# Optimization experiments

Measured on AMD Instinct MI355X. Metric: run time of the kernel, lower is better.

The kernel has to match this reference:

```python
import jax, jax.numpy as jnp
import numpy as np

B, S, H = 64, 2048, 1024

def setup_inputs() -> dict:
    key = jax.random.key(0)
    k1, k2 = jax.random.split(key)
    enc_output = jax.random.normal(k1, (B, S, H), dtype=jnp.float32)
    h_n = jax.random.normal(k2, (B, H), dtype=jnp.float32)
    return {"enc_output": enc_output, "h_n": h_n}

def reference(enc_output, h_n):
    # dec_output: [B, 1, H]
    dec_output = h_n[:, None, :]
    # scores: [B, 1, S] = dec_output @ enc_output^T
    scores = jnp.einsum('bqh,bsh->bqs', dec_output, enc_output)
    attn = jax.nn.softmax(scores, axis=2)  # softmax over S
    # context: [B, 1, H] = attn @ enc_output
    context = jnp.einsum('bqs,bsh->bqh', attn, enc_output)
    # concat decoder state and attention context: [B, 1, 2H]
    return jnp.concatenate((dec_output, context), axis=2)
```

## Files before the change

### kernel.cpp

```cpp
#include <hip/hip_runtime.h>
#include <math.h>


#define BB 64
#define SS 2048
#define HH 1024
#define NCHUNK 16
#define SCHUNK (SS / NCHUNK)
#define NWAVE 4

#define WS_ML_OFF ((size_t)BB * NCHUNK * HH)

__global__ __launch_bounds__(256) void attn_partial_kernel(
    const float* __restrict__ enc, const float* __restrict__ hn,
    float* __restrict__ ws)
{
    const int blk   = blockIdx.x;
    const int b     = blk / NCHUNK;
    const int chunk = blk % NCHUNK;
    const int tid   = threadIdx.x;
    const int wave  = tid >> 6;
    const int lane  = tid & 63;

    const float4* hn4 = (const float4*)(hn + (size_t)b * HH);
    float4 h4[4];
#pragma unroll
    for (int j = 0; j < 4; ++j) h4[j] = hn4[j * 64 + lane];

    const float4* enc4 = (const float4*)(enc + (size_t)b * SS * HH);

    float m = -INFINITY;
    float l = 0.0f;
    float4 acc[4];
#pragma unroll
    for (int j = 0; j < 4; ++j) acc[j] = make_float4(0.f, 0.f, 0.f, 0.f);

    const int s0 = chunk * SCHUNK;
    for (int s = s0 + wave; s < s0 + SCHUNK; s += NWAVE) {
        const float4* row = enc4 + (size_t)s * (HH / 4);
        float4 e[4];
#pragma unroll
        for (int j = 0; j < 4; ++j) e[j] = row[j * 64 + lane];

        float d = 0.0f;
#pragma unroll
        for (int j = 0; j < 4; ++j) {
            d += e[j].x * h4[j].x + e[j].y * h4[j].y
               + e[j].z * h4[j].z + e[j].w * h4[j].w;
        }
#pragma unroll
        for (int off = 32; off > 0; off >>= 1)
            d += __shfl_xor(d, off, 64);

        const float m_new = fmaxf(m, d);
        const float scale = __expf(m - m_new);
        const float p     = __expf(d - m_new);
        l = l * scale + p;
#pragma unroll
        for (int j = 0; j < 4; ++j) {
            acc[j].x = acc[j].x * scale + p * e[j].x;
            acc[j].y = acc[j].y * scale + p * e[j].y;
            acc[j].z = acc[j].z * scale + p * e[j].z;
            acc[j].w = acc[j].w * scale + p * e[j].w;
        }
        m = m_new;
    }

    __shared__ float s_m[NWAVE];
    __shared__ float s_l[NWAVE];
    __shared__ float s_acc[NWAVE][HH];

#pragma unroll
    for (int j = 0; j < 4; ++j)
        ((float4*)s_acc[wave])[j * 64 + lane] = acc[j];
    if (lane == 0) { s_m[wave] = m; s_l[wave] = l; }
    __syncthreads();

    float M = fmaxf(fmaxf(s_m[0], s_m[1]), fmaxf(s_m[2], s_m[3]));
    float sc[NWAVE];
    float L = 0.0f;
#pragma unroll
    for (int w = 0; w < NWAVE; ++w) {
        sc[w] = __expf(s_m[w] - M);
        L += s_l[w] * sc[w];
    }

    float4 ctx = make_float4(0.f, 0.f, 0.f, 0.f);
#pragma unroll
    for (int w = 0; w < NWAVE; ++w) {
        float4 a = ((const float4*)s_acc[w])[tid];
        ctx.x += sc[w] * a.x;  ctx.y += sc[w] * a.y;
        ctx.z += sc[w] * a.z;  ctx.w += sc[w] * a.w;
    }
    ((float4*)(ws + (size_t)blk * HH))[tid] = ctx;
    if (tid == 0) {
        ws[WS_ML_OFF + (size_t)blk * 2 + 0] = M;
        ws[WS_ML_OFF + (size_t)blk * 2 + 1] = L;
    }
}

__global__ __launch_bounds__(256) void attn_final_kernel(
    const float* __restrict__ hn, const float* __restrict__ ws,
    float* __restrict__ out)
{
    const int b   = blockIdx.x;
    const int tid = threadIdx.x;
    const float* ml = ws + WS_ML_OFF + (size_t)b * NCHUNK * 2;

    float M = -INFINITY;
#pragma unroll
    for (int c = 0; c < NCHUNK; ++c) M = fmaxf(M, ml[c * 2]);

    float sc[NCHUNK];
    float T = 0.0f;
#pragma unroll
    for (int c = 0; c < NCHUNK; ++c) {
        sc[c] = __expf(ml[c * 2] - M);
        T += sc[c] * ml[c * 2 + 1];
    }
    const float invT = 1.0f / T;

    float4 ctx = make_float4(0.f, 0.f, 0.f, 0.f);
#pragma unroll
    for (int c = 0; c < NCHUNK; ++c) {
        float4 a = ((const float4*)(ws + (size_t)(b * NCHUNK + c) * HH))[tid];
        ctx.x += sc[c] * a.x;  ctx.y += sc[c] * a.y;
        ctx.z += sc[c] * a.z;  ctx.w += sc[c] * a.w;
    }
    ctx.x *= invT; ctx.y *= invT; ctx.z *= invT; ctx.w *= invT;

    const float4 dec = ((const float4*)(hn + (size_t)b * HH))[tid];
    float4* o = (float4*)(out + (size_t)b * 2 * HH);
    o[tid]                = dec;
    o[tid + (HH / 4)]     = ctx;
}

extern "C" void kernel_launch(void* const* d_in, const int* in_sizes, int n_in,
                              void* d_out, int out_size, void* d_ws, size_t ws_size,
                              hipStream_t stream) {
    const float* enc = (const float*)d_in[0];
    const float* hn  = (const float*)d_in[1];
    float* out = (float*)d_out;
    float* ws  = (float*)d_ws;

    attn_partial_kernel<<<dim3(BB * NCHUNK), dim3(256), 0, stream>>>(enc, hn, ws);
    attn_final_kernel<<<dim3(BB), dim3(256), 0, stream>>>(hn, ws, out);
}
```

Measured before the change: 674.6 us.

## Batch four rows per wave in online softmax and double chunk count

Each wave now processes a contiguous run of rows in tiles of four. It issues all four rows' loads together, interleaves the four shuffle reductions, and does one rescale of the accumulator per tile instead of one per row. This is meant to raise memory-level parallelism and shorten the serial dependency chain in this bandwidth-bound kernel. The chunk count doubles to 32, giving 2048 blocks for more occupancy across CUs, at the cost of a larger partial workspace and more work in the final reduction. The extra per-tile registers may lower occupancy.

```diff
diff --git a/kernel.cpp b/kernel.cpp
--- a/kernel.cpp
+++ b/kernel.cpp
@@ -5,9 +5,12 @@
 #define BB 64
 #define SS 2048
 #define HH 1024
-#define NCHUNK 16
+#define NCHUNK 32
 #define SCHUNK (SS / NCHUNK)
 #define NWAVE 4
+#define RPW (SCHUNK / NWAVE)
+#define TT 4
+#define NTILE (RPW / TT)
 
 #define WS_ML_OFF ((size_t)BB * NCHUNK * HH)
 
@@ -35,33 +38,59 @@
 #pragma unroll
     for (int j = 0; j < 4; ++j) acc[j] = make_float4(0.f, 0.f, 0.f, 0.f);
 
-    const int s0 = chunk * SCHUNK;
-    for (int s = s0 + wave; s < s0 + SCHUNK; s += NWAVE) {
-        const float4* row = enc4 + (size_t)s * (HH / 4);
-        float4 e[4];
+    const int ws0 = chunk * SCHUNK + wave * RPW;
+
+    for (int t = 0; t < NTILE; ++t) {
+        const int sbase = ws0 + t * TT;
+
+        float4 e[TT][4];
 #pragma unroll
-        for (int j = 0; j < 4; ++j) e[j] = row[j * 64 + lane];
+        for (int r = 0; r < TT; ++r) {
+            const float4* row = enc4 + (size_t)(sbase + r) * (HH / 4);
+#pragma unroll
+            for (int j = 0; j < 4; ++j) e[r][j] = row[j * 64 + lane];
+        }
 
-        float d = 0.0f;
+        float d[TT];
+#pragma unroll
+        for (int r = 0; r < TT; ++r) {
+            float s = 0.0f;
+#pragma unroll
+            for (int j = 0; j < 4; ++j) {
+                s += e[r][j].x * h4[j].x + e[r][j].y * h4[j].y
+                   + e[r][j].z * h4[j].z + e[r][j].w * h4[j].w;
+            }
+            d[r] = s;
+        }
+
+#pragma unroll
+        for (int off = 32; off > 0; off >>= 1) {
+#pragma unroll
+            for (int r = 0; r < TT; ++r)
+                d[r] += __shfl_xor(d[r], off, 64);
+        }
+
+        float tmax = fmaxf(fmaxf(d[0], d[1]), fmaxf(d[2], d[3]));
+        const float m_new = fmaxf(m, tmax);
+        const float scale = __expf(m - m_new);
+        float p[TT];
+        float psum = 0.0f;
+#pragma unroll
+        for (int r = 0; r < TT; ++r) {
+            p[r] = __expf(d[r] - m_new);
+            psum += p[r];
+        }
+        l = l * scale + psum;
 #pragma unroll
         for (int j = 0; j < 4; ++j) {
-            d += e[j].x * h4[j].x + e[j].y * h4[j].y
-               + e[j].z * h4[j].z + e[j].w * h4[j].w;
-        }
+            float x = acc[j].x * scale, y = acc[j].y * scale;
+            float z = acc[j].z * scale, w = acc[j].w * scale;
 #pragma unroll
-        for (int off = 32; off > 0; off >>= 1)
-            d += __shfl_xor(d, off, 64);
-
-        const float m_new = fmaxf(m, d);
-        const float scale = __expf(m - m_new);
-        const float p     = __expf(d - m_new);
-        l = l * scale + p;
-#pragma unroll
-        for (int j = 0; j < 4; ++j) {
-            acc[j].x = acc[j].x * scale + p * e[j].x;
-            acc[j].y = acc[j].y * scale + p * e[j].y;
-            acc[j].z = acc[j].z * scale + p * e[j].z;
-            acc[j].w = acc[j].w * scale + p * e[j].w;
+            for (int r = 0; r < TT; ++r) {
+                x += p[r] * e[r][j].x;  y += p[r] * e[r][j].y;
+                z += p[r] * e[r][j].z;  w += p[r] * e[r][j].w;
+            }
+            acc[j] = make_float4(x, y, z, w);
         }
         m = m_new;
     }
@@ -131,8 +160,8 @@
 
     const float4 dec = ((const float4*)(hn + (size_t)b * HH))[tid];
     float4* o = (float4*)(out + (size_t)b * 2 * HH);
-    o[tid]                = dec;
-    o[tid + (HH / 4)]     = ctx;
+    o[tid]            = dec;
+    o[tid + (HH / 4)] = ctx;
 }
 
 extern "C" void kernel_launch(void* const* d_in, const int* in_sizes, int n_in,
```

Result: no change. 681.4 us (+1.0%).
